# Kernel tuning notes

Measured on AMD Instinct MI355X. Metric: run time of the kernel, lower is better.

Reference implementation:

```python
import jax, jax.numpy as jnp
import numpy as np
import math

D_MODEL = 1024
N_HEADS = 16
B, L, K = 2, 512, 4


def sinusoidal_pe(n, dim):
    # matches SinusoidalEmbedding buffer pe[:n]
    position = jnp.arange(n, dtype=jnp.float32)[:, None]
    div_term = jnp.exp(jnp.arange(0, dim, 2, dtype=jnp.float32) * (-math.log(10000.0) / dim))
    ang = position * div_term  # [n, dim//2]
    pe = jnp.zeros((n, dim), dtype=jnp.float32)
    pe = pe.at[:, 0::2].set(jnp.sin(ang))
    pe = pe.at[:, 1::2].set(jnp.cos(ang))
    return pe


def setup_inputs() -> dict:
    key = jax.random.key(0)
    ks = jax.random.split(key, 8)
    s = 1.0 / math.sqrt(D_MODEL)
    return {
        "h": jax.random.normal(ks[0], (B, L, K, D_MODEL), dtype=jnp.float32),
        "probs": jax.random.uniform(ks[1], (B, L, K), dtype=jnp.float32),
        "Wq": jax.random.normal(ks[2], (D_MODEL, D_MODEL), dtype=jnp.float32) * s,
        "bq": jnp.zeros((D_MODEL,), dtype=jnp.float32),
        "Wk": jax.random.normal(ks[3], (D_MODEL, D_MODEL), dtype=jnp.float32) * s,
        "bk": jnp.zeros((D_MODEL,), dtype=jnp.float32),
        "Wv": jax.random.normal(ks[4], (D_MODEL, D_MODEL), dtype=jnp.float32) * s,
        "bv": jnp.zeros((D_MODEL,), dtype=jnp.float32),
        "Wo": jax.random.normal(ks[5], (D_MODEL, D_MODEL), dtype=jnp.float32) * s,
        "bo": jnp.zeros((D_MODEL,), dtype=jnp.float32),
        "prob_bias_scale": jnp.float32(1.0),
        "n_heads": N_HEADS,
    }


def reference(h, probs, Wq, bq, Wk, bk, Wv, bv, Wo, bo, prob_bias_scale, n_heads):
    Bh, Lh, kh, D = h.shape
    N = Lh * kh
    hd = D // n_heads
    scale = hd ** (-0.5)

    h_flat = h.reshape(Bh, N, D) + sinusoidal_pe(N, D)[None]  # [B, N, D]
    probs_flat = probs.reshape(Bh, N)

    # torch Linear: x @ W.T + b
    q = (h_flat @ Wq.T + bq).reshape(Bh, N, n_heads, hd).transpose(0, 2, 1, 3)
    key = (h_flat @ Wk.T + bk).reshape(Bh, N, n_heads, hd).transpose(0, 2, 1, 3)
    v = (h_flat @ Wv.T + bv).reshape(Bh, N, n_heads, hd).transpose(0, 2, 1, 3)

    scores = jnp.einsum("bhnd,bhmd->bhnm", q, key) * scale  # [B,H,N,N]
    prob_bias = jnp.log(probs_flat + 1e-8)[:, None, None, :]  # bias on key axis
    scores = scores + prob_bias_scale * prob_bias
    attn = jax.nn.softmax(scores, axis=-1)  # dropout is identity in eval
    out = jnp.einsum("bhnm,bhmd->bhnd", attn, v)
    out = out.transpose(0, 2, 1, 3).reshape(Bh, N, D)
    out = out @ Wo.T + bo
    return out.reshape(Bh, Lh, kh, D)
```

## Files before the change

kernel.cpp:

```cpp
#include <hip/hip_runtime.h>

typedef _Float16 h8 __attribute__((ext_vector_type(8)));
typedef _Float16 h4 __attribute__((ext_vector_type(4)));
typedef __fp16 fp16x2 __attribute__((ext_vector_type(2)));
typedef float f32x4 __attribute__((ext_vector_type(4)));

#define NSEQ 2048
#define DMODEL 1024
#define HD 64
#define C2 0.1803368801111244f

#define OFF_HPE  (size_t)0
#define OFF_WQ   (size_t)8388608
#define OFF_WK   (size_t)10485760
#define OFF_WV   (size_t)12582912
#define OFF_WO   (size_t)14680064
#define OFF_Q    (size_t)16777216
#define OFF_K    (size_t)25165824
#define OFF_VT   (size_t)33554432
#define OFF_AO   (size_t)41943040
#define OFF_PB   (size_t)50331648

#define GLL(g, l) __builtin_amdgcn_global_load_lds( \
    (const __attribute__((address_space(1))) unsigned int*)(const void*)(g), \
    (__attribute__((address_space(3))) unsigned int*)(l), 16, 0, 0)

__global__ void hpe_kernel(const float* __restrict__ h, _Float16* __restrict__ hpe) {
    int idx = blockIdx.x * blockDim.x + threadIdx.x;
    int row = idx >> 7;
    int c8 = (idx & 127) * 8;
    int n = row & (NSEQ - 1);
    const float kL = -0.025952563241307517f;
    const float kInv2Pi = 0.15915494309189535f;
    union { float4 f4[2]; float f[8]; } in;
    in.f4[0] = *(const float4*)&h[(size_t)row * DMODEL + c8];
    in.f4[1] = *(const float4*)&h[(size_t)row * DMODEL + c8 + 4];
    union { _Float16 hh[8]; uint4 u; } out;
    #pragma unroll
    for (int p = 0; p < 4; ++p) {
        int i2 = (c8 >> 1) + p;
        float div = __builtin_amdgcn_exp2f((float)i2 * kL);
        float rev = (float)n * div * kInv2Pi;
        float rf = __builtin_amdgcn_fractf(rev);
        float s = __builtin_amdgcn_sinf(rf);
        float c = __builtin_amdgcn_cosf(rf);
        out.hh[2 * p]     = (_Float16)(in.f[2 * p] + s);
        out.hh[2 * p + 1] = (_Float16)(in.f[2 * p + 1] + c);
    }
    *(uint4*)&hpe[(size_t)row * DMODEL + c8] = out.u;
}

__global__ void cast4_kernel(const float* __restrict__ w0, const float* __restrict__ w1,
                             const float* __restrict__ w2, const float* __restrict__ w3,
                             _Float16* __restrict__ d0, _Float16* __restrict__ d1,
                             _Float16* __restrict__ d2, _Float16* __restrict__ d3) {
    int i = blockIdx.x * blockDim.x + threadIdx.x;
    int which = i >> 18, idx = i & 262143;
    const float* s = which == 0 ? w0 : which == 1 ? w1 : which == 2 ? w2 : w3;
    _Float16* d    = which == 0 ? d0 : which == 1 ? d1 : which == 2 ? d2 : d3;
    float sc = which == 0 ? C2 : 1.0f;
    float4 v = ((const float4*)s)[idx];
    union { _Float16 hh[4]; uint2 u; } o;
    o.hh[0] = (_Float16)(v.x * sc); o.hh[1] = (_Float16)(v.y * sc);
    o.hh[2] = (_Float16)(v.z * sc); o.hh[3] = (_Float16)(v.w * sc);
    ((uint2*)d)[idx] = o.u;
}

__global__ void pb_kernel(const float* __restrict__ probs, const float* __restrict__ pbs,
                          float* __restrict__ pb) {
    int i = blockIdx.x * blockDim.x + threadIdx.x;
    pb[i] = pbs[0] * log2f(probs[i] + 1e-8f);
}

__global__ __launch_bounds__(256) void gemm_qkv(
    const _Float16* __restrict__ A,
    const _Float16* __restrict__ Wqp, const _Float16* __restrict__ Wkp, const _Float16* __restrict__ Wvp,
    const float* __restrict__ bqp, const float* __restrict__ bkp, const float* __restrict__ bvp,
    _Float16* __restrict__ qb, _Float16* __restrict__ kb, _Float16* __restrict__ vt)
{
    __shared__ __align__(16) _Float16 As[128][64];
    __shared__ __align__(16) _Float16 Bs[128][64];
    int widx = blockIdx.y >> 3;
    const _Float16* W = widx == 0 ? Wqp : widx == 1 ? Wkp : Wvp;
    const float* bias = widx == 0 ? bqp : widx == 1 ? bkp : bvp;
    float bscale = widx == 0 ? C2 : 1.0f;
    int tm = blockIdx.x * 128;
    int tn = (blockIdx.y & 7) * 128;
    int t = threadIdx.x;
    int wave = t >> 6, lane = t & 63;
    int wr = (wave >> 1) * 64, wc = (wave & 1) * 64;
    int lr = lane & 15, lg = lane >> 4;

    f32x4 acc[4][4] = {};

    int grow = lane >> 3;
    int gcol = (lane & 7) * 8;
    const _Float16* Aptr = A + (size_t)(tm + wave * 8 + grow) * DMODEL + gcol;
    const _Float16* Wptr = W + (size_t)(tn + wave * 8 + grow) * DMODEL + gcol;

    for (int k0 = 0; k0 < DMODEL; k0 += 64) {
        __syncthreads();
        #pragma unroll
        for (int i = 0; i < 4; ++i)
            GLL(Aptr + (size_t)i * 32 * DMODEL + k0, &As[i * 32 + wave * 8][0]);
        #pragma unroll
        for (int i = 0; i < 4; ++i)
            GLL(Wptr + (size_t)i * 32 * DMODEL + k0, &Bs[i * 32 + wave * 8][0]);
        __syncthreads();
        #pragma unroll
        for (int kk = 0; kk < 2; ++kk) {
            h8 af[4], bf[4];
            #pragma unroll
            for (int mi = 0; mi < 4; ++mi) af[mi] = *(const h8*)&As[wr + mi * 16 + lr][kk * 32 + lg * 8];
            #pragma unroll
            for (int ni = 0; ni < 4; ++ni) bf[ni] = *(const h8*)&Bs[wc + ni * 16 + lr][kk * 32 + lg * 8];
            #pragma unroll
            for (int mi = 0; mi < 4; ++mi)
                #pragma unroll
                for (int ni = 0; ni < 4; ++ni)
                    acc[mi][ni] = __builtin_amdgcn_mfma_f32_16x16x32_f16(af[mi], bf[ni], acc[mi][ni], 0, 0, 0);
        }
    }

    #pragma unroll
    for (int mi = 0; mi < 4; ++mi)
        #pragma unroll
        for (int ni = 0; ni < 4; ++ni) {
            int col = tn + wc + ni * 16 + lr;
            float bv = bias[col] * bscale;
            if (widx < 2) {
                _Float16* dst = widx == 0 ? qb : kb;
                #pragma unroll
                for (int j = 0; j < 4; ++j) {
                    int row = tm + wr + mi * 16 + lg * 4 + j;
                    dst[(size_t)row * DMODEL + col] = (_Float16)(acc[mi][ni][j] + bv);
                }
            } else {
                int row0 = tm + wr + mi * 16 + lg * 4;
                int b = row0 >> 11, n0 = row0 & 2047;
                h4 pk;
                #pragma unroll
                for (int j = 0; j < 4; ++j) pk[j] = (_Float16)(acc[mi][ni][j] + bv);
                *(h4*)&vt[((size_t)b * 1024 + col) * 2048 + n0] = pk;
            }
        }
}

__global__ __launch_bounds__(256) void gemm_ao(
    const _Float16* __restrict__ A, const _Float16* __restrict__ W,
    const float* __restrict__ bias, float* __restrict__ C)
{
    __shared__ __align__(16) _Float16 As[64][64];
    __shared__ __align__(16) _Float16 Bs[128][64];
    int tm = blockIdx.x * 64;
    int tn = blockIdx.y * 128;
    int t = threadIdx.x;
    int wave = t >> 6, lane = t & 63;
    int wr = (wave >> 1) * 32, wc = (wave & 1) * 64;
    int lr = lane & 15, lg = lane >> 4;

    f32x4 acc[2][4] = {};

    int grow = lane >> 3;
    int gcol = (lane & 7) * 8;
    const _Float16* Aptr = A + (size_t)(tm + wave * 8 + grow) * DMODEL + gcol;
    const _Float16* Wptr = W + (size_t)(tn + wave * 8 + grow) * DMODEL + gcol;

    for (int k0 = 0; k0 < DMODEL; k0 += 64) {
        __syncthreads();
        #pragma unroll
        for (int i = 0; i < 2; ++i)
            GLL(Aptr + (size_t)i * 32 * DMODEL + k0, &As[i * 32 + wave * 8][0]);
        #pragma unroll
        for (int i = 0; i < 4; ++i)
            GLL(Wptr + (size_t)i * 32 * DMODEL + k0, &Bs[i * 32 + wave * 8][0]);
        __syncthreads();
        #pragma unroll
        for (int kk = 0; kk < 2; ++kk) {
            h8 af[2], bf[4];
            #pragma unroll
            for (int mi = 0; mi < 2; ++mi) af[mi] = *(const h8*)&As[wr + mi * 16 + lr][kk * 32 + lg * 8];
            #pragma unroll
            for (int ni = 0; ni < 4; ++ni) bf[ni] = *(const h8*)&Bs[wc + ni * 16 + lr][kk * 32 + lg * 8];
            #pragma unroll
            for (int mi = 0; mi < 2; ++mi)
                #pragma unroll
                for (int ni = 0; ni < 4; ++ni)
                    acc[mi][ni] = __builtin_amdgcn_mfma_f32_16x16x32_f16(af[mi], bf[ni], acc[mi][ni], 0, 0, 0);
        }
    }

    #pragma unroll
    for (int mi = 0; mi < 2; ++mi)
        #pragma unroll
        for (int ni = 0; ni < 4; ++ni)
            #pragma unroll
            for (int j = 0; j < 4; ++j) {
                int row = tm + wr + mi * 16 + lg * 4 + j;
                int col = tn + wc + ni * 16 + lr;
                C[(size_t)row * DMODEL + col] = acc[mi][ni][j] + bias[col];
            }
}

#define QT 64
#define KT 64

#define SWZ(row, bytecol) ((row) * 128 + ((bytecol) ^ (((row) & 7) << 4)))

__global__ __launch_bounds__(256, 4) void flash_kernel(
    const _Float16* __restrict__ Qb,
    const _Float16* __restrict__ Kb,
    const _Float16* __restrict__ Vt,
    const float* __restrict__ pb,
    _Float16* __restrict__ AO)
{
    __shared__ __align__(16) char KsB[64 * 128];
    __shared__ __align__(16) char VsB[64 * 128];
    __shared__ __align__(16) _Float16 Ps[4][16][72];
    int bh = blockIdx.y;
    int b = bh >> 4, h = bh & 15;
    int q0 = blockIdx.x * QT;
    int t = threadIdx.x, wave = t >> 6, lane = t & 63;
    int lr = lane & 15, lg = lane >> 4;

    const _Float16* Khead  = Kb + (size_t)b * NSEQ * DMODEL + h * HD;
    const _Float16* Vthead = Vt + ((size_t)b * 1024 + h * HD) * NSEQ;
    const float* pbb = pb + b * NSEQ;

    const _Float16* Qrow = Qb + ((size_t)b * NSEQ + q0 + wave * 16 + lr) * DMODEL + h * HD;
    h8 qf0 = *(const h8*)&Qrow[lg * 8];
    h8 qf1 = *(const h8*)&Qrow[32 + lg * 8];

    const h8 vones = { (_Float16)1, (_Float16)1, (_Float16)1, (_Float16)1,
                       (_Float16)1, (_Float16)1, (_Float16)1, (_Float16)1 };

    float mrun = -INFINITY;
    f32x4 oacc[4] = {};
    f32x4 lsum = {};

    int srow = t >> 2;
    int sc = (t & 3) * 32;

    for (int k0 = 0; k0 < NSEQ; k0 += KT) {
        f32x4 s[4];
        #pragma unroll
        for (int ci = 0; ci < 4; ++ci)
            s[ci] = *(const f32x4*)&pbb[k0 + ci * 16 + lg * 4];

        __syncthreads();
        *(h8*)(KsB + SWZ(srow, sc))      = *(const h8*)&Khead[(size_t)(k0 + srow) * DMODEL + (sc >> 1)];
        *(h8*)(KsB + SWZ(srow, sc + 16)) = *(const h8*)&Khead[(size_t)(k0 + srow) * DMODEL + (sc >> 1) + 8];
        *(h8*)(VsB + SWZ(srow, sc))      = *(const h8*)&Vthead[(size_t)srow * NSEQ + k0 + (sc >> 1)];
        *(h8*)(VsB + SWZ(srow, sc + 16)) = *(const h8*)&Vthead[(size_t)srow * NSEQ + k0 + (sc >> 1) + 8];
        __syncthreads();

        #pragma unroll
        for (int ci = 0; ci < 4; ++ci) {
            h8 kf = *(const h8*)(KsB + SWZ(ci * 16 + lr, lg * 16));
            s[ci] = __builtin_amdgcn_mfma_f32_16x16x32_f16(kf, qf0, s[ci], 0, 0, 0);
        }
        #pragma unroll
        for (int ci = 0; ci < 4; ++ci) {
            h8 kf = *(const h8*)(KsB + SWZ(ci * 16 + lr, 64 + lg * 16));
            s[ci] = __builtin_amdgcn_mfma_f32_16x16x32_f16(kf, qf1, s[ci], 0, 0, 0);
        }

        float sm = s[0][0];
        #pragma unroll
        for (int ci = 0; ci < 4; ++ci)
            #pragma unroll
            for (int j = 0; j < 4; ++j) sm = fmaxf(sm, s[ci][j]);
        sm = fmaxf(sm, __shfl_xor(sm, 16));
        sm = fmaxf(sm, __shfl_xor(sm, 32));

        bool need = __any(sm > mrun);
        float newm = need ? fmaxf(mrun, sm) : mrun;

        #pragma unroll
        for (int ci = 0; ci < 4; ++ci) {
            fp16x2 a = __builtin_amdgcn_cvt_pkrtz(__builtin_amdgcn_exp2f(s[ci][0] - newm),
                                                  __builtin_amdgcn_exp2f(s[ci][1] - newm));
            fp16x2 b2 = __builtin_amdgcn_cvt_pkrtz(__builtin_amdgcn_exp2f(s[ci][2] - newm),
                                                   __builtin_amdgcn_exp2f(s[ci][3] - newm));
            union { fp16x2 hh[2]; uint2 u; } pk;
            pk.hh[0] = a; pk.hh[1] = b2;
            *(uint2*)&Ps[wave][lr][ci * 16 + lg * 4] = pk.u;
        }

        h8 vf[2][4];
        #pragma unroll
        for (int kb = 0; kb < 2; ++kb)
            #pragma unroll
            for (int ni = 0; ni < 4; ++ni)
                vf[kb][ni] = *(const h8*)(VsB + SWZ(ni * 16 + lr, kb * 64 + lg * 16));

        if (need) {
            float fs = __builtin_amdgcn_exp2f(mrun - newm);
            mrun = newm;
            #pragma unroll
            for (int j = 0; j < 4; ++j) {
                float fsj = __shfl(fs, (lane & 48) | (lg * 4 + j), 64);
                #pragma unroll
                for (int ni = 0; ni < 4; ++ni) oacc[ni][j] *= fsj;
                lsum[j] *= fsj;
            }
        }

        asm volatile("s_waitcnt lgkmcnt(0)" ::: "memory");

        #pragma unroll
        for (int kb = 0; kb < 2; ++kb) {
            h8 pa = *(const h8*)&Ps[wave][lr][kb * 32 + lg * 8];
            #pragma unroll
            for (int ni = 0; ni < 4; ++ni)
                oacc[ni] = __builtin_amdgcn_mfma_f32_16x16x32_f16(pa, vf[kb][ni], oacc[ni], 0, 0, 0);
            lsum = __builtin_amdgcn_mfma_f32_16x16x32_f16(pa, vones, lsum, 0, 0, 0);
        }
    }

    #pragma unroll
    for (int j = 0; j < 4; ++j) {
        float inv = 1.0f / lsum[j];
        int row = q0 + wave * 16 + lg * 4 + j;
        #pragma unroll
        for (int ni = 0; ni < 4; ++ni)
            AO[((size_t)b * NSEQ + row) * DMODEL + h * HD + ni * 16 + lr] = (_Float16)(oacc[ni][j] * inv);
    }
}

extern "C" void kernel_launch(void* const* d_in, const int* in_sizes, int n_in,
                              void* d_out, int out_size, void* d_ws, size_t ws_size,
                              hipStream_t stream) {
    const float* h    = (const float*)d_in[0];
    const float* prob = (const float*)d_in[1];
    const float* Wq   = (const float*)d_in[2];
    const float* bq   = (const float*)d_in[3];
    const float* Wk   = (const float*)d_in[4];
    const float* bk   = (const float*)d_in[5];
    const float* Wv   = (const float*)d_in[6];
    const float* bv   = (const float*)d_in[7];
    const float* Wo   = (const float*)d_in[8];
    const float* bo   = (const float*)d_in[9];
    const float* pbs  = (const float*)d_in[10];

    char* ws = (char*)d_ws;
    _Float16* hpe  = (_Float16*)(ws + OFF_HPE);
    _Float16* wq16 = (_Float16*)(ws + OFF_WQ);
    _Float16* wk16 = (_Float16*)(ws + OFF_WK);
    _Float16* wv16 = (_Float16*)(ws + OFF_WV);
    _Float16* wo16 = (_Float16*)(ws + OFF_WO);
    _Float16* qb   = (_Float16*)(ws + OFF_Q);
    _Float16* kb16 = (_Float16*)(ws + OFF_K);
    _Float16* vt   = (_Float16*)(ws + OFF_VT);
    _Float16* ao   = (_Float16*)(ws + OFF_AO);
    float*    pbuf = (float*)(ws + OFF_PB);

    hpe_kernel<<<dim3(2048), dim3(256), 0, stream>>>(h, hpe);
    cast4_kernel<<<dim3(4096), dim3(256), 0, stream>>>(Wq, Wk, Wv, Wo, wq16, wk16, wv16, wo16);
    pb_kernel<<<dim3(16), dim3(256), 0, stream>>>(prob, pbs, pbuf);

    gemm_qkv<<<dim3(32, 24), dim3(256), 0, stream>>>(hpe, wq16, wk16, wv16, bq, bk, bv, qb, kb16, vt);

    flash_kernel<<<dim3(32, 32), dim3(256), 0, stream>>>(qb, kb16, vt, pbuf, ao);

    gemm_ao<<<dim3(64, 8), dim3(256), 0, stream>>>(ao, wo16, bo, (float*)d_out);
}
```

Baseline: 246.1 us.

## Double-buffer flash K/V tiles with async LDS loads, bigger blocks, XCD-aware block remap

The flash kernel now uses 512-thread blocks covering 128 queries. K/V tiles are double-buffered in LDS and filled with global_load_lds prefetches of the next tile, replacing the synchronous load-store path with one barrier per iteration. A swizzled chunk index keeps the bank-conflict-free layout. All three main kernels also remap block IDs so consecutive blocks on the same XCD share tiles, aiming at better L2 reuse, at the cost of more LDS per block and possibly lower occupancy.

Result: faster. 233.8 us (-5.0%).

```diff
diff --git a/kernel.cpp b/kernel.cpp
--- a/kernel.cpp
+++ b/kernel.cpp
@@ -80,12 +80,15 @@
 {
     __shared__ __align__(16) _Float16 As[128][64];
     __shared__ __align__(16) _Float16 Bs[128][64];
-    int widx = blockIdx.y >> 3;
+    int bid = blockIdx.x + 32 * blockIdx.y;
+    int nf = (bid & 7) * 96 + (bid >> 3);
+    int bx = nf & 31, byy = nf >> 5;
+    int widx = byy >> 3;
     const _Float16* W = widx == 0 ? Wqp : widx == 1 ? Wkp : Wvp;
     const float* bias = widx == 0 ? bqp : widx == 1 ? bkp : bvp;
     float bscale = widx == 0 ? C2 : 1.0f;
-    int tm = blockIdx.x * 128;
-    int tn = (blockIdx.y & 7) * 128;
+    int tm = bx * 128;
+    int tn = (byy & 7) * 128;
     int t = threadIdx.x;
     int wave = t >> 6, lane = t & 63;
     int wr = (wave >> 1) * 64, wc = (wave & 1) * 64;
@@ -152,8 +155,10 @@
 {
     __shared__ __align__(16) _Float16 As[64][64];
     __shared__ __align__(16) _Float16 Bs[128][64];
-    int tm = blockIdx.x * 64;
-    int tn = blockIdx.y * 128;
+    int bid = blockIdx.x + 64 * blockIdx.y;
+    int nf = (bid & 7) * 64 + (bid >> 3);
+    int tm = (nf & 63) * 64;
+    int tn = (nf >> 6) * 128;
     int t = threadIdx.x;
     int wave = t >> 6, lane = t & 63;
     int wr = (wave >> 1) * 32, wc = (wave & 1) * 64;
@@ -202,24 +207,26 @@
             }
 }
 
-#define QT 64
 #define KT 64
 
 #define SWZ(row, bytecol) ((row) * 128 + ((bytecol) ^ (((row) & 7) << 4)))
 
-__global__ __launch_bounds__(256, 4) void flash_kernel(
+__global__ __launch_bounds__(512) void flash_kernel(
     const _Float16* __restrict__ Qb,
     const _Float16* __restrict__ Kb,
     const _Float16* __restrict__ Vt,
     const float* __restrict__ pb,
     _Float16* __restrict__ AO)
 {
-    __shared__ __align__(16) char KsB[64 * 128];
-    __shared__ __align__(16) char VsB[64 * 128];
-    __shared__ __align__(16) _Float16 Ps[4][16][72];
-    int bh = blockIdx.y;
+    __shared__ __align__(16) char KsB[2][8192];
+    __shared__ __align__(16) char VsB[2][8192];
+    __shared__ __align__(16) _Float16 Ps[8][16][72];
+
+    int bid = blockIdx.x + 16 * blockIdx.y;
+    int nf = (bid & 7) * 64 + (bid >> 3);
+    int qx = nf & 15, bh = nf >> 4;
     int b = bh >> 4, h = bh & 15;
-    int q0 = blockIdx.x * QT;
+    int q0 = qx * 128;
     int t = threadIdx.x, wave = t >> 6, lane = t & 63;
     int lr = lane & 15, lg = lane >> 4;
 
@@ -238,30 +245,38 @@
     f32x4 oacc[4] = {};
     f32x4 lsum = {};
 
-    int srow = t >> 2;
-    int sc = (t & 3) * 32;
-
-    for (int k0 = 0; k0 < NSEQ; k0 += KT) {
+    int srow = t >> 3;
+    int schunk = (t & 7) ^ (srow & 7);
+    const _Float16* Ksrc = Khead + (size_t)srow * DMODEL + schunk * 8;
+    const _Float16* Vsrc = Vthead + (size_t)srow * NSEQ + schunk * 8;
+
+    GLL(Ksrc, KsB[0] + wave * 1024);
+    GLL(Vsrc, VsB[0] + wave * 1024);
+    asm volatile("s_waitcnt vmcnt(0)" ::: "memory");
+    __syncthreads();
+
+    int cur = 0;
+    for (int kt = 0; kt < 32; ++kt) {
+        int k0 = kt * KT;
+        if (kt < 31) {
+            GLL(Ksrc + (size_t)(k0 + KT) * DMODEL, KsB[cur ^ 1] + wave * 1024);
+            GLL(Vsrc + (k0 + KT), VsB[cur ^ 1] + wave * 1024);
+        }
+        const char* Kc = KsB[cur];
+        const char* Vc = VsB[cur];
+
         f32x4 s[4];
         #pragma unroll
         for (int ci = 0; ci < 4; ++ci)
             s[ci] = *(const f32x4*)&pbb[k0 + ci * 16 + lg * 4];
-
-        __syncthreads();
-        *(h8*)(KsB + SWZ(srow, sc))      = *(const h8*)&Khead[(size_t)(k0 + srow) * DMODEL + (sc >> 1)];
-        *(h8*)(KsB + SWZ(srow, sc + 16)) = *(const h8*)&Khead[(size_t)(k0 + srow) * DMODEL + (sc >> 1) + 8];
-        *(h8*)(VsB + SWZ(srow, sc))      = *(const h8*)&Vthead[(size_t)srow * NSEQ + k0 + (sc >> 1)];
-        *(h8*)(VsB + SWZ(srow, sc + 16)) = *(const h8*)&Vthead[(size_t)srow * NSEQ + k0 + (sc >> 1) + 8];
-        __syncthreads();
-
         #pragma unroll
         for (int ci = 0; ci < 4; ++ci) {
-            h8 kf = *(const h8*)(KsB + SWZ(ci * 16 + lr, lg * 16));
+            h8 kf = *(const h8*)(Kc + SWZ(ci * 16 + lr, lg * 16));
             s[ci] = __builtin_amdgcn_mfma_f32_16x16x32_f16(kf, qf0, s[ci], 0, 0, 0);
         }
         #pragma unroll
         for (int ci = 0; ci < 4; ++ci) {
-            h8 kf = *(const h8*)(KsB + SWZ(ci * 16 + lr, 64 + lg * 16));
+            h8 kf = *(const h8*)(Kc + SWZ(ci * 16 + lr, 64 + lg * 16));
             s[ci] = __builtin_amdgcn_mfma_f32_16x16x32_f16(kf, qf1, s[ci], 0, 0, 0);
         }
 
@@ -292,7 +307,7 @@
         for (int kb = 0; kb < 2; ++kb)
             #pragma unroll
             for (int ni = 0; ni < 4; ++ni)
-                vf[kb][ni] = *(const h8*)(VsB + SWZ(ni * 16 + lr, kb * 64 + lg * 16));
+                vf[kb][ni] = *(const h8*)(Vc + SWZ(ni * 16 + lr, kb * 64 + lg * 16));
 
         if (need) {
             float fs = __builtin_amdgcn_exp2f(mrun - newm);
@@ -307,6 +322,7 @@
         }
 
         asm volatile("s_waitcnt lgkmcnt(0)" ::: "memory");
+        __builtin_amdgcn_sched_barrier(0);
 
         #pragma unroll
         for (int kb = 0; kb < 2; ++kb) {
@@ -316,6 +332,10 @@
                 oacc[ni] = __builtin_amdgcn_mfma_f32_16x16x32_f16(pa, vf[kb][ni], oacc[ni], 0, 0, 0);
             lsum = __builtin_amdgcn_mfma_f32_16x16x32_f16(pa, vones, lsum, 0, 0, 0);
         }
+
+        asm volatile("s_waitcnt vmcnt(0)" ::: "memory");
+        __syncthreads();
+        cur ^= 1;
     }
 
     #pragma unroll
@@ -361,7 +381,7 @@
 
     gemm_qkv<<<dim3(32, 24), dim3(256), 0, stream>>>(hpe, wq16, wk16, wv16, bq, bk, bv, qb, kb16, vt);
 
-    flash_kernel<<<dim3(32, 32), dim3(256), 0, stream>>>(qb, kb16, vt, pbuf, ao);
+    flash_kernel<<<dim3(16, 32), dim3(512), 0, stream>>>(qb, kb16, vt, pbuf, ao);
 
     gemm_ao<<<dim3(64, 8), dim3(256), 0, stream>>>(ao, wo16, bo, (float*)d_out);
 }
```
